# Kernel optimization log

Hardware: AMD Instinct MI355X
Metric: run time of the kernel (lower is better)

Reference implementation:

```python
import jax, jax.numpy as jnp
import numpy as np

N, IN_DIM, OUT_DIM = 8192, 512, 256


def setup_inputs() -> dict:
    key = jax.random.key(0)
    k1, k2, k3 = jax.random.split(key, 3)
    X = jax.random.normal(k1, (N, IN_DIM), dtype=jnp.float32)
    # torch nn.Linear(in_dim, out_dim, bias=False): y = x @ W^T; store as [in_dim, out_dim]
    W = jax.random.normal(k2, (IN_DIM, OUT_DIM), dtype=jnp.float32) / np.sqrt(IN_DIM)
    # a: Linear(2*out_dim, 1, bias=False) -> vector of length 2*out_dim
    a = jax.random.normal(k3, (2 * OUT_DIM,), dtype=jnp.float32) / np.sqrt(2 * OUT_DIM)
    return {"X": X, "W": W, "a": a}


def reference(X, W, a):
    H = X @ W  # [N, D]
    D = H.shape[1]
    # a([Hi ; Hj]) = Hi @ a[:D] + Hj @ a[D:] -> avoid materializing [N,N,2D]
    e = (H @ a[:D])[:, None] + (H @ a[D:])[None, :]  # [N, N]
    e = jnp.where(e > 0, e, 0.2 * e)  # leaky_relu(0.2)
    A = jax.nn.softmax(e, axis=-1)  # row softmax [N, N]
    out = A @ H  # [N, D]
    return out, A
```

## Files before the change

kernel.cpp:

```cpp
#include <hip/hip_runtime.h>
#include <math.h>

#define NN 8192
#define KDIM 512
#define DD 256
#define CS 32
#define NC 256

typedef float4 f4;
typedef __attribute__((ext_vector_type(4))) float f4v;

__device__ __forceinline__ float dot4(const f4& x, const f4& y) {
  return x.x * y.x + x.y * y.y + x.z * y.z + x.w * y.w;
}

__global__ __launch_bounds__(256) void k_gemm(const float* __restrict__ X,
                                              const float* __restrict__ W,
                                              const float* __restrict__ av,
                                              float* __restrict__ H,
                                              float* __restrict__ s,
                                              float* __restrict__ t) {
  __shared__ float Xs[32][64];
  __shared__ float Ws[32][64];
  const int tid = threadIdx.x;
  const int tx = tid & 15;
  const int ty = tid >> 4;
  const int r0 = blockIdx.x * 64;
  const int c0 = blockIdx.y * 64;
  float acc[4][4] = {};
  for (int k0 = 0; k0 < KDIM; k0 += 32) {
#pragma unroll
    for (int q = 0; q < 2; ++q) {
      int fi = tid + q * 256;
      int r = fi >> 3;
      int kq = fi & 7;
      f4 v = *reinterpret_cast<const f4*>(&X[(size_t)(r0 + r) * KDIM + k0 + kq * 4]);
      Xs[kq * 4 + 0][r] = v.x; Xs[kq * 4 + 1][r] = v.y;
      Xs[kq * 4 + 2][r] = v.z; Xs[kq * 4 + 3][r] = v.w;
    }
#pragma unroll
    for (int q = 0; q < 2; ++q) {
      int fi = tid + q * 256;
      int k = fi >> 4;
      int cq = fi & 15;
      *reinterpret_cast<f4*>(&Ws[k][cq * 4]) =
          *reinterpret_cast<const f4*>(&W[(size_t)(k0 + k) * DD + c0 + cq * 4]);
    }
    __syncthreads();
#pragma unroll
    for (int k = 0; k < 32; ++k) {
      f4 xv = *reinterpret_cast<const f4*>(&Xs[k][ty * 4]);
      f4 wv = *reinterpret_cast<const f4*>(&Ws[k][tx * 4]);
      float xs[4] = {xv.x, xv.y, xv.z, xv.w};
      float ws[4] = {wv.x, wv.y, wv.z, wv.w};
#pragma unroll
      for (int i = 0; i < 4; ++i)
#pragma unroll
        for (int j = 0; j < 4; ++j) acc[i][j] += xs[i] * ws[j];
    }
    __syncthreads();
  }
#pragma unroll
  for (int i = 0; i < 4; ++i) {
    f4 v = {acc[i][0], acc[i][1], acc[i][2], acc[i][3]};
    *reinterpret_cast<f4*>(&H[(size_t)(r0 + ty * 4 + i) * DD + c0 + tx * 4]) = v;
  }

  if (c0 == 0) {
    int wid = tid >> 6, lane = tid & 63;
    float* wv1 = &Xs[0][0];
    float* wv2 = &Xs[0][0] + 512;
    for (int k = tid; k < KDIM; k += 256) {
      float a1acc = 0.f, a2acc = 0.f;
#pragma unroll 8
      for (int d4 = 0; d4 < DD / 4; ++d4) {
        f4 wrow = *reinterpret_cast<const f4*>(&W[(size_t)k * DD + d4 * 4]);
        f4 a1v = *reinterpret_cast<const f4*>(&av[d4 * 4]);
        f4 a2v = *reinterpret_cast<const f4*>(&av[DD + d4 * 4]);
        a1acc += dot4(wrow, a1v);
        a2acc += dot4(wrow, a2v);
      }
      wv1[k] = a1acc;
      wv2[k] = a2acc;
    }
    __syncthreads();
    f4 w1a = *reinterpret_cast<const f4*>(&wv1[lane * 8]);
    f4 w1b = *reinterpret_cast<const f4*>(&wv1[lane * 8 + 4]);
    f4 w2a = *reinterpret_cast<const f4*>(&wv2[lane * 8]);
    f4 w2b = *reinterpret_cast<const f4*>(&wv2[lane * 8 + 4]);
    for (int rr = 0; rr < 16; ++rr) {
      int i = r0 + wid * 16 + rr;
      f4 xa = *reinterpret_cast<const f4*>(&X[(size_t)i * KDIM + lane * 8]);
      f4 xb = *reinterpret_cast<const f4*>(&X[(size_t)i * KDIM + lane * 8 + 4]);
      float p1 = dot4(xa, w1a) + dot4(xb, w1b);
      float p2 = dot4(xa, w2a) + dot4(xb, w2b);
      for (int off = 32; off > 0; off >>= 1) {
        p1 += __shfl_down(p1, off);
        p2 += __shfl_down(p2, off);
      }
      if (lane == 0) { s[i] = p1; t[i] = p2; }
    }
  }
}

__global__ __launch_bounds__(256) void k_mid(const float* __restrict__ s,
                                             const float* __restrict__ t,
                                             float* __restrict__ E1,
                                             float* __restrict__ E2,
                                             float* __restrict__ c1,
                                             float* __restrict__ c2,
                                             float* __restrict__ tsort,
                                             int* __restrict__ perm,
                                             float* __restrict__ Es1,
                                             float* __restrict__ Es2,
                                             int* __restrict__ kidx) {
  __shared__ float lred[4];
  const int b = blockIdx.x, tid = threadIdx.x;
  const int wid = tid >> 6, lane = tid & 63;
  float m = -1e30f;
#pragma unroll
  for (int q = 0; q < 8; ++q) {
    int idx = (q * 256 + tid) * 4;
    f4 v = *reinterpret_cast<const f4*>(&t[idx]);
    m = fmaxf(m, fmaxf(fmaxf(v.x, v.y), fmaxf(v.z, v.w)));
  }
  for (int off = 32; off > 0; off >>= 1) m = fmaxf(m, __shfl_down(m, off));
  if (lane == 0) lred[wid] = m;
  __syncthreads();
  float tmax = fmaxf(fmaxf(lred[0], lred[1]), fmaxf(lred[2], lred[3]));

  if (tid < 16) {
    int i = b * 16 + tid;
    float ti = t[i];
    E1[i] = expf(ti);
    E2[i] = expf(0.2f * ti);
    float si = s[i];
    float e = si + tmax;
    float mm = e > 0.f ? e : 0.2f * e;
    c1[i] = expf(si - mm);
    c2[i] = expf(0.2f * si - mm);
  }

  float tkv[4], skv[4]; int jj[4], cnt[4], cntk[4];
#pragma unroll
  for (int q = 0; q < 4; ++q) {
    jj[q] = b * 16 + wid * 4 + q;
    tkv[q] = t[jj[q]];
    skv[q] = -s[jj[q]];
    cnt[q] = 0;
    cntk[q] = 0;
  }
  for (int m2 = 0; m2 < 32; ++m2) {
    int i4 = m2 * 64 + lane;
    f4 v = *reinterpret_cast<const f4*>(&t[i4 * 4]);
    int base = i4 * 4;
#pragma unroll
    for (int q = 0; q < 4; ++q) {
      cnt[q] += (v.x < tkv[q]) || (v.x == tkv[q] && base + 0 < jj[q]);
      cnt[q] += (v.y < tkv[q]) || (v.y == tkv[q] && base + 1 < jj[q]);
      cnt[q] += (v.z < tkv[q]) || (v.z == tkv[q] && base + 2 < jj[q]);
      cnt[q] += (v.w < tkv[q]) || (v.w == tkv[q] && base + 3 < jj[q]);
      cntk[q] += (v.x <= skv[q]) + (v.y <= skv[q]) + (v.z <= skv[q]) + (v.w <= skv[q]);
    }
  }
#pragma unroll
  for (int q = 0; q < 4; ++q) {
    int c = cnt[q], ck = cntk[q];
    for (int off = 32; off > 0; off >>= 1) {
      c += __shfl_down(c, off);
      ck += __shfl_down(ck, off);
    }
    if (lane == 0) {
      tsort[c] = tkv[q];
      perm[c] = jj[q];
      Es1[c] = expf(tkv[q]);
      Es2[c] = expf(0.2f * tkv[q]);
      kidx[jj[q]] = ck;
    }
  }
}

__global__ __launch_bounds__(256) void k_chunk(const float* __restrict__ H,
                                               const float* __restrict__ Es1,
                                               const float* __restrict__ Es2,
                                               const int* __restrict__ perm,
                                               float* __restrict__ Hs,
                                               float* __restrict__ Ctot1,
                                               float* __restrict__ Ctot2,
                                               float* __restrict__ cs1,
                                               float* __restrict__ cs2) {
  __shared__ int pms[CS];
  int c = blockIdx.x;
  int d = threadIdx.x;
  if (d < CS) pms[d] = perm[c * CS + d];
  __syncthreads();
  float s1 = 0.f, s2 = 0.f, a1 = 0.f, a2 = 0.f;
#pragma unroll 4
  for (int kk = 0; kk < CS; ++kk) {
    int mI = c * CS + kk;
    float e1 = Es1[mI], e2 = Es2[mI];
    float h = H[(size_t)pms[kk] * DD + d];
    Hs[(size_t)mI * DD + d] = h;
    s1 += e1 * h; s2 += e2 * h;
    a1 += e1;     a2 += e2;
  }
  Ctot1[c * DD + d] = s1;
  Ctot2[c * DD + d] = s2;
  if (d == 0) { cs1[c] = a1; cs2[c] = a2; }
}

__global__ __launch_bounds__(256) void k_scan(const float* __restrict__ Ctot1,
                                              const float* __restrict__ Ctot2,
                                              const float* __restrict__ cs1,
                                              const float* __restrict__ cs2,
                                              const float* __restrict__ Es1,
                                              const float* __restrict__ Es2,
                                              const int* __restrict__ kidx,
                                              const float* __restrict__ c1,
                                              const float* __restrict__ c2,
                                              float* __restrict__ Cpre1,
                                              float* __restrict__ Cpre2,
                                              float* __restrict__ f1,
                                              float* __restrict__ f2) {
  __shared__ float sc1[NC], sc2[NC];
  const int c = blockIdx.x;
  const int d = threadIdx.x;
  float r1a = 0.f, r1b = 0.f, r2a = 0.f, r2b = 0.f;
  int cc = 0;
  for (; cc + 4 <= c; cc += 4) {
    r1a += Ctot1[(cc + 0) * DD + d];
    r1b += Ctot1[(cc + 1) * DD + d];
    r1a += Ctot1[(cc + 2) * DD + d];
    r1b += Ctot1[(cc + 3) * DD + d];
    r2a += Ctot2[(cc + 0) * DD + d];
    r2b += Ctot2[(cc + 1) * DD + d];
    r2a += Ctot2[(cc + 2) * DD + d];
    r2b += Ctot2[(cc + 3) * DD + d];
  }
  for (; cc < c; ++cc) {
    r1a += Ctot1[cc * DD + d];
    r2a += Ctot2[cc * DD + d];
  }
  float r1 = r1a + r1b, r2 = r2a + r2b;
  Cpre1[(size_t)c * DD + d] = r1;
  Cpre2[(size_t)c * DD + d] = r2;
  if (c == NC - 1) {
    Cpre1[(size_t)NC * DD + d] = r1 + Ctot1[c * DD + d];
    Cpre2[(size_t)NC * DD + d] = r2 + Ctot2[c * DD + d];
  }
  sc1[d] = cs1[d];
  sc2[d] = cs2[d];
  __syncthreads();
  for (int off = 1; off < NC; off <<= 1) {
    float y1 = (d >= off) ? sc1[d - off] : 0.f;
    float y2 = (d >= off) ? sc2[d - off] : 0.f;
    __syncthreads();
    sc1[d] += y1; sc2[d] += y2;
    __syncthreads();
  }
  if (d < 32) {
    int i = c * 32 + d;
    int ki = kidx[i];
    int ci = ki >> 5;
    float sp1 = ci ? sc1[ci - 1] : 0.f;
    float sp2 = ci ? sc2[ci - 1] : 0.f;
    for (int m = ci * CS; m < ki; ++m) { sp1 += Es1[m]; sp2 += Es2[m]; }
    float T1s = sc1[NC - 1];
    float a1 = c1[i], a2 = c2[i];
    float Z = a1 * (T1s - sp1) + a2 * sp2;
    float rZ = 1.0f / Z;
    f1[i] = rZ * a1;
    f2[i] = rZ * a2;
  }
}

__global__ __launch_bounds__(256) void k_fin2(const int* __restrict__ kidx,
                                              const float* __restrict__ Es1,
                                              const float* __restrict__ Es2,
                                              const float* __restrict__ Hs,
                                              const float* __restrict__ Cpre1,
                                              const float* __restrict__ Cpre2,
                                              const float* __restrict__ f1,
                                              const float* __restrict__ f2,
                                              float* __restrict__ out) {
  const int b = blockIdx.x;
  const int d = threadIdx.x;
  float T1 = Cpre1[(size_t)NC * DD + d];
#pragma unroll
  for (int r = 0; r < 4; ++r) {
    int i = b * 4 + r;
    int ki = kidx[i];
    int ci = ki >> 5;
    float P1 = Cpre1[(size_t)ci * DD + d];
    float P2 = Cpre2[(size_t)ci * DD + d];
    for (int m = ci * CS; m < ki; ++m) {
      float h = Hs[(size_t)m * DD + d];
      P1 += Es1[m] * h;
      P2 += Es2[m] * h;
    }
    out[(size_t)i * DD + d] = f1[i] * (T1 - P1) + f2[i] * P2;
  }
}

__global__ __launch_bounds__(256) void k_astream(const float* __restrict__ s,
                                                 const float* __restrict__ t,
                                                 const float* __restrict__ E1,
                                                 const float* __restrict__ E2,
                                                 const float* __restrict__ f1,
                                                 const float* __restrict__ f2,
                                                 float* __restrict__ A) {
  int j0 = blockIdx.x * 1024 + threadIdx.x * 4;
  int i0 = blockIdx.y * 32;
  f4 t4  = *reinterpret_cast<const f4*>(&t[j0]);
  f4 e14 = *reinterpret_cast<const f4*>(&E1[j0]);
  f4 e24 = *reinterpret_cast<const f4*>(&E2[j0]);
#pragma unroll 4
  for (int rr = 0; rr < 32; ++rr) {
    int i = i0 + rr;
    float ss = s[i], ff1 = f1[i], ff2 = f2[i];
    f4v o;
    float e;
    e = ss + t4.x; o.x = (e > 0.f) ? ff1 * e14.x : ff2 * e24.x;
    e = ss + t4.y; o.y = (e > 0.f) ? ff1 * e14.y : ff2 * e24.y;
    e = ss + t4.z; o.z = (e > 0.f) ? ff1 * e14.z : ff2 * e24.z;
    e = ss + t4.w; o.w = (e > 0.f) ? ff1 * e14.w : ff2 * e24.w;
    __builtin_nontemporal_store(o, reinterpret_cast<f4v*>(&A[(size_t)i * NN + j0]));
  }
}

extern "C" void kernel_launch(void* const* d_in, const int* in_sizes, int n_in,
                              void* d_out, int out_size, void* d_ws, size_t ws_size,
                              hipStream_t stream) {
  const float* X  = (const float*)d_in[0];
  const float* W  = (const float*)d_in[1];
  const float* av = (const float*)d_in[2];
  float* outp = (float*)d_out;
  float* A = outp + (size_t)NN * DD;

  float* wsp = (float*)d_ws;
  float* s  = wsp + 0 * NN;
  float* t  = wsp + 1 * NN;
  float* E1 = wsp + 2 * NN;
  float* E2 = wsp + 3 * NN;
  float* c1 = wsp + 4 * NN;
  float* c2 = wsp + 5 * NN;
  float* f1 = wsp + 6 * NN;
  float* f2 = wsp + 7 * NN;

  float* Ctot1 = A;
  float* Ctot2 = A + 65536;
  float* Cpre1 = A + 131072;
  float* Cpre2 = A + 196864;
  float* cs1   = A + 262656;
  float* cs2   = A + 262912;
  float* tsort = A + 263168;
  int*   perm  = (int*)(A + 271360);
  int*   kidx  = (int*)(A + 279552);
  float* Es1   = A + 287744;
  float* Es2   = A + 295936;
  float* H     = A + 16777216;
  float* Hs    = A + 20971520;

  k_gemm<<<dim3(NN / 64, DD / 64), 256, 0, stream>>>(X, W, av, H, s, t);
  k_mid<<<NN / 16, 256, 0, stream>>>(s, t, E1, E2, c1, c2, tsort, perm,
                                     Es1, Es2, kidx);
  k_chunk<<<NC, 256, 0, stream>>>(H, Es1, Es2, perm, Hs, Ctot1, Ctot2, cs1, cs2);
  k_scan<<<NC, 256, 0, stream>>>(Ctot1, Ctot2, cs1, cs2, Es1, Es2, kidx, c1, c2,
                                 Cpre1, Cpre2, f1, f2);
  k_fin2<<<NN / 4, 256, 0, stream>>>(kidx, Es1, Es2, Hs, Cpre1, Cpre2, f1, f2, outp);
  k_astream<<<dim3(NN / 1024, NN / 32), 256, 0, stream>>>(s, t, E1, E2, f1, f2, A);
}
```

Measured before the change: 197.6 us.

## Fuse final output and attention-matrix stream kernels, drop sorted H copy

Removes the permuted copy Hs and the unused tsort writes, so the final pass gathers H rows through perm instead. When the workspace is large enough, scratch buffers move from the A output region into the workspace, which lets the output-row computation and the A-matrix streaming store run in a single fused kernel. The goal is to cut an 8 MB copy and one launch, and to overlap the gather-heavy output rows with the bandwidth-bound A stream. The cost is indirect, less coalesced H reads in the tail loop, plus an unfused fallback path when the workspace is small.

```diff
diff --git a/kernel.cpp b/kernel.cpp
--- a/kernel.cpp
+++ b/kernel.cpp
@@ -109,7 +109,6 @@
                                              float* __restrict__ E2,
                                              float* __restrict__ c1,
                                              float* __restrict__ c2,
-                                             float* __restrict__ tsort,
                                              int* __restrict__ perm,
                                              float* __restrict__ Es1,
                                              float* __restrict__ Es2,
@@ -171,7 +170,6 @@
       ck += __shfl_down(ck, off);
     }
     if (lane == 0) {
-      tsort[c] = tkv[q];
       perm[c] = jj[q];
       Es1[c] = expf(tkv[q]);
       Es2[c] = expf(0.2f * tkv[q]);
@@ -184,7 +182,6 @@
                                                const float* __restrict__ Es1,
                                                const float* __restrict__ Es2,
                                                const int* __restrict__ perm,
-                                               float* __restrict__ Hs,
                                                float* __restrict__ Ctot1,
                                                float* __restrict__ Ctot2,
                                                float* __restrict__ cs1,
@@ -200,7 +197,6 @@
     int mI = c * CS + kk;
     float e1 = Es1[mI], e2 = Es2[mI];
     float h = H[(size_t)pms[kk] * DD + d];
-    Hs[(size_t)mI * DD + d] = h;
     s1 += e1 * h; s2 += e2 * h;
     a1 += e1;     a2 += e2;
   }
@@ -274,27 +270,27 @@
   }
 }
 
-__global__ __launch_bounds__(256) void k_fin2(const int* __restrict__ kidx,
-                                              const float* __restrict__ Es1,
-                                              const float* __restrict__ Es2,
-                                              const float* __restrict__ Hs,
-                                              const float* __restrict__ Cpre1,
-                                              const float* __restrict__ Cpre2,
-                                              const float* __restrict__ f1,
-                                              const float* __restrict__ f2,
-                                              float* __restrict__ out) {
-  const int b = blockIdx.x;
-  const int d = threadIdx.x;
+__device__ __forceinline__ void fin_rows(int i0, int d,
+                                         const int* __restrict__ kidx,
+                                         const float* __restrict__ Es1,
+                                         const float* __restrict__ Es2,
+                                         const int* __restrict__ perm,
+                                         const float* __restrict__ H,
+                                         const float* __restrict__ Cpre1,
+                                         const float* __restrict__ Cpre2,
+                                         const float* __restrict__ f1,
+                                         const float* __restrict__ f2,
+                                         float* __restrict__ out) {
   float T1 = Cpre1[(size_t)NC * DD + d];
 #pragma unroll
   for (int r = 0; r < 4; ++r) {
-    int i = b * 4 + r;
+    int i = i0 + r;
     int ki = kidx[i];
     int ci = ki >> 5;
     float P1 = Cpre1[(size_t)ci * DD + d];
     float P2 = Cpre2[(size_t)ci * DD + d];
     for (int m = ci * CS; m < ki; ++m) {
-      float h = Hs[(size_t)m * DD + d];
+      float h = H[(size_t)perm[m] * DD + d];
       P1 += Es1[m] * h;
       P2 += Es2[m] * h;
     }
@@ -302,15 +298,14 @@
   }
 }
 
-__global__ __launch_bounds__(256) void k_astream(const float* __restrict__ s,
-                                                 const float* __restrict__ t,
-                                                 const float* __restrict__ E1,
-                                                 const float* __restrict__ E2,
-                                                 const float* __restrict__ f1,
-                                                 const float* __restrict__ f2,
-                                                 float* __restrict__ A) {
-  int j0 = blockIdx.x * 1024 + threadIdx.x * 4;
-  int i0 = blockIdx.y * 32;
+__device__ __forceinline__ void astream_tile(int i0, int j0,
+                                             const float* __restrict__ s,
+                                             const float* __restrict__ t,
+                                             const float* __restrict__ E1,
+                                             const float* __restrict__ E2,
+                                             const float* __restrict__ f1,
+                                             const float* __restrict__ f2,
+                                             float* __restrict__ A) {
   f4 t4  = *reinterpret_cast<const f4*>(&t[j0]);
   f4 e14 = *reinterpret_cast<const f4*>(&E1[j0]);
   f4 e24 = *reinterpret_cast<const f4*>(&E2[j0]);
@@ -328,6 +323,52 @@
   }
 }
 
+__global__ __launch_bounds__(256) void k_finstream(const int* __restrict__ kidx,
+                                                   const float* __restrict__ Es1,
+                                                   const float* __restrict__ Es2,
+                                                   const int* __restrict__ perm,
+                                                   const float* __restrict__ H,
+                                                   const float* __restrict__ Cpre1,
+                                                   const float* __restrict__ Cpre2,
+                                                   const float* __restrict__ f1,
+                                                   const float* __restrict__ f2,
+                                                   float* __restrict__ out,
+                                                   const float* __restrict__ s,
+                                                   const float* __restrict__ t,
+                                                   const float* __restrict__ E1,
+                                                   const float* __restrict__ E2,
+                                                   float* __restrict__ A) {
+  const int bb = blockIdx.x;
+  const int d = threadIdx.x;
+  fin_rows(bb * 4, d, kidx, Es1, Es2, perm, H, Cpre1, Cpre2, f1, f2, out);
+  astream_tile((bb >> 3) * 32, (bb & 7) * 1024 + d * 4, s, t, E1, E2, f1, f2, A);
+}
+
+__global__ __launch_bounds__(256) void k_fin2(const int* __restrict__ kidx,
+                                              const float* __restrict__ Es1,
+                                              const float* __restrict__ Es2,
+                                              const int* __restrict__ perm,
+                                              const float* __restrict__ H,
+                                              const float* __restrict__ Cpre1,
+                                              const float* __restrict__ Cpre2,
+                                              const float* __restrict__ f1,
+                                              const float* __restrict__ f2,
+                                              float* __restrict__ out) {
+  fin_rows(blockIdx.x * 4, threadIdx.x, kidx, Es1, Es2, perm, H, Cpre1, Cpre2,
+           f1, f2, out);
+}
+
+__global__ __launch_bounds__(256) void k_astream(const float* __restrict__ s,
+                                                 const float* __restrict__ t,
+                                                 const float* __restrict__ E1,
+                                                 const float* __restrict__ E2,
+                                                 const float* __restrict__ f1,
+                                                 const float* __restrict__ f2,
+                                                 float* __restrict__ A) {
+  astream_tile(blockIdx.y * 32, blockIdx.x * 1024 + threadIdx.x * 4,
+               s, t, E1, E2, f1, f2, A);
+}
+
 extern "C" void kernel_launch(void* const* d_in, const int* in_sizes, int n_in,
                               void* d_out, int out_size, void* d_ws, size_t ws_size,
                               hipStream_t stream) {
@@ -336,8 +377,8 @@
   const float* av = (const float*)d_in[2];
   float* outp = (float*)d_out;
   float* A = outp + (size_t)NN * DD;
-
   float* wsp = (float*)d_ws;
+
   float* s  = wsp + 0 * NN;
   float* t  = wsp + 1 * NN;
   float* E1 = wsp + 2 * NN;
@@ -347,26 +388,47 @@
   float* f1 = wsp + 6 * NN;
   float* f2 = wsp + 7 * NN;
 
-  float* Ctot1 = A;
-  float* Ctot2 = A + 65536;
-  float* Cpre1 = A + 131072;
-  float* Cpre2 = A + 196864;
-  float* cs1   = A + 262656;
-  float* cs2   = A + 262912;
-  float* tsort = A + 263168;
-  int*   perm  = (int*)(A + 271360);
-  int*   kidx  = (int*)(A + 279552);
-  float* Es1   = A + 287744;
-  float* Es2   = A + 295936;
-  float* H     = A + 16777216;
-  float* Hs    = A + 20971520;
-
-  k_gemm<<<dim3(NN / 64, DD / 64), 256, 0, stream>>>(X, W, av, H, s, t);
-  k_mid<<<NN / 16, 256, 0, stream>>>(s, t, E1, E2, c1, c2, tsort, perm,
-                                     Es1, Es2, kidx);
-  k_chunk<<<NC, 256, 0, stream>>>(H, Es1, Es2, perm, Hs, Ctot1, Ctot2, cs1, cs2);
-  k_scan<<<NC, 256, 0, stream>>>(Ctot1, Ctot2, cs1, cs2, Es1, Es2, kidx, c1, c2,
-                                 Cpre1, Cpre2, f1, f2);
-  k_fin2<<<NN / 4, 256, 0, stream>>>(kidx, Es1, Es2, Hs, Cpre1, Cpre2, f1, f2, outp);
-  k_astream<<<dim3(NN / 1024, NN / 32), 256, 0, stream>>>(s, t, E1, E2, f1, f2, A);
-}
+  const size_t FAST_WS_FLOATS = 393216 + (size_t)NN * DD;
+  if (ws_size >= FAST_WS_FLOATS * sizeof(float)) {
+    float* Ctot1 = wsp + 65536;
+    float* Ctot2 = wsp + 131072;
+    float* Cpre1 = wsp + 196608;
+    float* Cpre2 = wsp + 262400;
+    float* cs1   = wsp + 328192;
+    float* cs2   = wsp + 328448;
+    float* Es1   = wsp + 328704;
+    float* Es2   = wsp + 336896;
+    int*   kidx  = (int*)(wsp + 345088);
+    int*   perm  = (int*)(wsp + 353280);
+    float* H     = wsp + 393216;
+
+    k_gemm<<<dim3(NN / 64, DD / 64), 256, 0, stream>>>(X, W, av, H, s, t);
+    k_mid<<<NN / 16, 256, 0, stream>>>(s, t, E1, E2, c1, c2, perm, Es1, Es2, kidx);
+    k_chunk<<<NC, 256, 0, stream>>>(H, Es1, Es2, perm, Ctot1, Ctot2, cs1, cs2);
+    k_scan<<<NC, 256, 0, stream>>>(Ctot1, Ctot2, cs1, cs2, Es1, Es2, kidx, c1, c2,
+                                   Cpre1, Cpre2, f1, f2);
+    k_finstream<<<NN / 4, 256, 0, stream>>>(kidx, Es1, Es2, perm, H, Cpre1, Cpre2,
+                                            f1, f2, outp, s, t, E1, E2, A);
+  } else {
+    float* Ctot1 = A;
+    float* Ctot2 = A + 65536;
+    float* Cpre1 = A + 131072;
+    float* Cpre2 = A + 196864;
+    float* cs1   = A + 262656;
+    float* cs2   = A + 262912;
+    int*   perm  = (int*)(A + 271360);
+    int*   kidx  = (int*)(A + 279552);
+    float* Es1   = A + 287744;
+    float* Es2   = A + 295936;
+    float* H     = A + 16777216;
+
+    k_gemm<<<dim3(NN / 64, DD / 64), 256, 0, stream>>>(X, W, av, H, s, t);
+    k_mid<<<NN / 16, 256, 0, stream>>>(s, t, E1, E2, c1, c2, perm, Es1, Es2, kidx);
+    k_chunk<<<NC, 256, 0, stream>>>(H, Es1, Es2, perm, Ctot1, Ctot2, cs1, cs2);
+    k_scan<<<NC, 256, 0, stream>>>(Ctot1, Ctot2, cs1, cs2, Es1, Es2, kidx, c1, c2,
+                                   Cpre1, Cpre2, f1, f2);
+    k_fin2<<<NN / 4, 256, 0, stream>>>(kidx, Es1, Es2, perm, H, Cpre1, Cpre2,
+                                       f1, f2, outp);
+    k_astream<<<dim3(NN / 1024, NN / 32), 256, 0, stream>>>(s, t, E1, E2, f1, f2, A);
+  }
+}
```

Result: faster. 183.5 us (median of 2 runs) (-7.2%).

## Replace rank-count sort with value-bucketed histogram and fuse output with A stream

Applied to the files above, without the earlier changes.

Swaps the O(N^2) rank-counting sort of t for value-range bucketing into 256 buckets, each sorted locally by one block from a shared-memory copy of t. The same block also gathers H and computes per-bucket weighted totals, merging the old mid and chunk kernels. The output-row kernel and the A-writing stream kernel become one launch, and scratch moves from the A region into the workspace. Bucket sizes now depend on the data, so a skewed distribution can overflow the 2048-entry bucket list and cause uneven per-block work.

```diff
diff --git a/kernel.cpp b/kernel.cpp
--- a/kernel.cpp
+++ b/kernel.cpp
@@ -4,14 +4,18 @@
 #define NN 8192
 #define KDIM 512
 #define DD 256
-#define CS 32
-#define NC 256
+#define NCB 256
 
 typedef float4 f4;
 typedef __attribute__((ext_vector_type(4))) float f4v;
 
 __device__ __forceinline__ float dot4(const f4& x, const f4& y) {
   return x.x * y.x + x.y * y.y + x.z * y.z + x.w * y.w;
+}
+
+__device__ __forceinline__ int bk(float x, float tmin, float sc) {
+  int b = (int)floorf((x - tmin) * sc);
+  return b < 0 ? 0 : (b > NCB - 1 ? NCB - 1 : b);
 }
 
 __global__ __launch_bounds__(256) void k_gemm(const float* __restrict__ X,
@@ -103,35 +107,59 @@
   }
 }
 
-__global__ __launch_bounds__(256) void k_mid(const float* __restrict__ s,
-                                             const float* __restrict__ t,
-                                             float* __restrict__ E1,
-                                             float* __restrict__ E2,
-                                             float* __restrict__ c1,
-                                             float* __restrict__ c2,
-                                             float* __restrict__ tsort,
-                                             int* __restrict__ perm,
-                                             float* __restrict__ Es1,
-                                             float* __restrict__ Es2,
-                                             int* __restrict__ kidx) {
-  __shared__ float lred[4];
-  const int b = blockIdx.x, tid = threadIdx.x;
+__global__ __launch_bounds__(256) void k_vtot(const float* __restrict__ s,
+                                              const float* __restrict__ t,
+                                              const float* __restrict__ H,
+                                              float* __restrict__ E1,
+                                              float* __restrict__ E2,
+                                              float* __restrict__ c1,
+                                              float* __restrict__ c2,
+                                              float* __restrict__ Vtot1,
+                                              float* __restrict__ Vtot2,
+                                              float* __restrict__ Vcs1,
+                                              float* __restrict__ Vcs2,
+                                              float* __restrict__ tz,
+                                              float* __restrict__ Ez1,
+                                              float* __restrict__ Ez2,
+                                              float* __restrict__ Hs,
+                                              int* __restrict__ boffg,
+                                              int* __restrict__ cntg,
+                                              float* __restrict__ tmm) {
+  __shared__ float ts[NN];
+  __shared__ int hist[NCB];
+  __shared__ int sh1[NCB];
+  __shared__ int tcnt[256];
+  __shared__ int sh2[256];
+  __shared__ int mlist[2048];
+  __shared__ int srt[2048];
+  __shared__ float lred[4], lredn[4];
+  const int c = blockIdx.x, tid = threadIdx.x;
   const int wid = tid >> 6, lane = tid & 63;
-  float m = -1e30f;
+
+  float mx = -1e30f, mn = 1e30f;
 #pragma unroll
   for (int q = 0; q < 8; ++q) {
     int idx = (q * 256 + tid) * 4;
     f4 v = *reinterpret_cast<const f4*>(&t[idx]);
-    m = fmaxf(m, fmaxf(fmaxf(v.x, v.y), fmaxf(v.z, v.w)));
-  }
-  for (int off = 32; off > 0; off >>= 1) m = fmaxf(m, __shfl_down(m, off));
-  if (lane == 0) lred[wid] = m;
+    *reinterpret_cast<f4*>(&ts[idx]) = v;
+    mx = fmaxf(mx, fmaxf(fmaxf(v.x, v.y), fmaxf(v.z, v.w)));
+    mn = fminf(mn, fminf(fminf(v.x, v.y), fminf(v.z, v.w)));
+  }
+  for (int off = 32; off > 0; off >>= 1) {
+    mx = fmaxf(mx, __shfl_down(mx, off));
+    mn = fminf(mn, __shfl_down(mn, off));
+  }
+  if (lane == 0) { lred[wid] = mx; lredn[wid] = mn; }
   __syncthreads();
   float tmax = fmaxf(fmaxf(lred[0], lred[1]), fmaxf(lred[2], lred[3]));
-
-  if (tid < 16) {
-    int i = b * 16 + tid;
-    float ti = t[i];
+  float tmin = fminf(fminf(lredn[0], lredn[1]), fminf(lredn[2], lredn[3]));
+  float range = tmax - tmin;
+  float sc = (range > 0.f) ? (float)NCB / range : 0.f;
+  if (c == 0 && tid == 0) { tmm[0] = tmin; tmm[1] = sc; }
+
+  if (tid < 32) {
+    int i = c * 32 + tid;
+    float ti = ts[i];
     E1[i] = expf(ti);
     E2[i] = expf(0.2f * ti);
     float si = s[i];
@@ -141,117 +169,125 @@
     c2[i] = expf(0.2f * si - mm);
   }
 
-  float tkv[4], skv[4]; int jj[4], cnt[4], cntk[4];
-#pragma unroll
-  for (int q = 0; q < 4; ++q) {
-    jj[q] = b * 16 + wid * 4 + q;
-    tkv[q] = t[jj[q]];
-    skv[q] = -s[jj[q]];
-    cnt[q] = 0;
-    cntk[q] = 0;
-  }
-  for (int m2 = 0; m2 < 32; ++m2) {
-    int i4 = m2 * 64 + lane;
-    f4 v = *reinterpret_cast<const f4*>(&t[i4 * 4]);
-    int base = i4 * 4;
-#pragma unroll
-    for (int q = 0; q < 4; ++q) {
-      cnt[q] += (v.x < tkv[q]) || (v.x == tkv[q] && base + 0 < jj[q]);
-      cnt[q] += (v.y < tkv[q]) || (v.y == tkv[q] && base + 1 < jj[q]);
-      cnt[q] += (v.z < tkv[q]) || (v.z == tkv[q] && base + 2 < jj[q]);
-      cnt[q] += (v.w < tkv[q]) || (v.w == tkv[q] && base + 3 < jj[q]);
-      cntk[q] += (v.x <= skv[q]) + (v.y <= skv[q]) + (v.z <= skv[q]) + (v.w <= skv[q]);
-    }
-  }
-#pragma unroll
-  for (int q = 0; q < 4; ++q) {
-    int c = cnt[q], ck = cntk[q];
-    for (int off = 32; off > 0; off >>= 1) {
-      c += __shfl_down(c, off);
-      ck += __shfl_down(ck, off);
-    }
-    if (lane == 0) {
-      tsort[c] = tkv[q];
-      perm[c] = jj[q];
-      Es1[c] = expf(tkv[q]);
-      Es2[c] = expf(0.2f * tkv[q]);
-      kidx[jj[q]] = ck;
-    }
-  }
-}
-
-__global__ __launch_bounds__(256) void k_chunk(const float* __restrict__ H,
-                                               const float* __restrict__ Es1,
-                                               const float* __restrict__ Es2,
-                                               const int* __restrict__ perm,
-                                               float* __restrict__ Hs,
-                                               float* __restrict__ Ctot1,
-                                               float* __restrict__ Ctot2,
-                                               float* __restrict__ cs1,
-                                               float* __restrict__ cs2) {
-  __shared__ int pms[CS];
-  int c = blockIdx.x;
-  int d = threadIdx.x;
-  if (d < CS) pms[d] = perm[c * CS + d];
-  __syncthreads();
-  float s1 = 0.f, s2 = 0.f, a1 = 0.f, a2 = 0.f;
-#pragma unroll 4
-  for (int kk = 0; kk < CS; ++kk) {
-    int mI = c * CS + kk;
-    float e1 = Es1[mI], e2 = Es2[mI];
-    float h = H[(size_t)pms[kk] * DD + d];
-    Hs[(size_t)mI * DD + d] = h;
-    s1 += e1 * h; s2 += e2 * h;
-    a1 += e1;     a2 += e2;
-  }
-  Ctot1[c * DD + d] = s1;
-  Ctot2[c * DD + d] = s2;
-  if (d == 0) { cs1[c] = a1; cs2[c] = a2; }
-}
-
-__global__ __launch_bounds__(256) void k_scan(const float* __restrict__ Ctot1,
-                                              const float* __restrict__ Ctot2,
-                                              const float* __restrict__ cs1,
-                                              const float* __restrict__ cs2,
-                                              const float* __restrict__ Es1,
-                                              const float* __restrict__ Es2,
-                                              const int* __restrict__ kidx,
+  hist[tid] = 0;
+  __syncthreads();
+  int myc = 0;
+  for (int k = 0; k < 32; ++k) {
+    int j = tid * 32 + k;
+    int b = bk(ts[j], tmin, sc);
+    atomicAdd(&hist[b], 1);
+    myc += (b == c);
+  }
+  tcnt[tid] = myc;
+  __syncthreads();
+  int h0 = hist[tid], tc0 = tcnt[tid];
+  sh1[tid] = h0; sh2[tid] = tc0;
+  __syncthreads();
+  for (int off = 1; off < 256; off <<= 1) {
+    int a1 = (tid >= off) ? sh1[tid - off] : 0;
+    int a2 = (tid >= off) ? sh2[tid - off] : 0;
+    __syncthreads();
+    sh1[tid] += a1; sh2[tid] += a2;
+    __syncthreads();
+  }
+  const int boffc = (c > 0) ? sh1[c - 1] : 0;
+  const int nm = hist[c];
+  const int tb = sh2[tid] - tc0;
+  if (tid == 0) { boffg[c] = boffc; cntg[c] = nm; }
+
+  int w = 0;
+  for (int k = 0; k < 32; ++k) {
+    int j = tid * 32 + k;
+    if (bk(ts[j], tmin, sc) == c) {
+      int slot = tb + w;
+      if (slot < 2048) mlist[slot] = j;
+      ++w;
+    }
+  }
+  __syncthreads();
+
+  for (int k = tid; k < nm; k += 256) {
+    int j = mlist[k];
+    float v = ts[j];
+    int r = 0;
+    for (int k2 = 0; k2 < nm; ++k2) {
+      int j2 = mlist[k2];
+      float v2 = ts[j2];
+      r += (v2 < v) || (v2 == v && j2 < j);
+    }
+    srt[r] = j;
+  }
+  __syncthreads();
+
+  float a1 = 0.f, a2 = 0.f, scs1 = 0.f, scs2 = 0.f;
+  for (int r2 = 0; r2 < nm; ++r2) {
+    int j = srt[r2];
+    float tv = ts[j];
+    float e1 = expf(tv), e2 = expf(0.2f * tv);
+    float hv = H[(size_t)j * DD + tid];
+    Hs[(size_t)(boffc + r2) * DD + tid] = hv;
+    a1 += e1 * hv;
+    a2 += e2 * hv;
+    if (tid == 0) {
+      tz[boffc + r2] = tv;
+      Ez1[boffc + r2] = e1;
+      Ez2[boffc + r2] = e2;
+      scs1 += e1;
+      scs2 += e2;
+    }
+  }
+  Vtot1[c * DD + tid] = a1;
+  Vtot2[c * DD + tid] = a2;
+  if (tid == 0) { Vcs1[c] = scs1; Vcs2[c] = scs2; }
+}
+
+__global__ __launch_bounds__(256) void k_scan(const float* __restrict__ Vtot1,
+                                              const float* __restrict__ Vtot2,
+                                              const float* __restrict__ Vcs1,
+                                              const float* __restrict__ Vcs2,
+                                              const float* __restrict__ tz,
+                                              const float* __restrict__ Ez1,
+                                              const float* __restrict__ Ez2,
+                                              const int* __restrict__ boffg,
+                                              const int* __restrict__ cntg,
+                                              const float* __restrict__ tmm,
+                                              const float* __restrict__ s,
                                               const float* __restrict__ c1,
                                               const float* __restrict__ c2,
-                                              float* __restrict__ Cpre1,
-                                              float* __restrict__ Cpre2,
+                                              float* __restrict__ Vpre1,
+                                              float* __restrict__ Vpre2,
                                               float* __restrict__ f1,
                                               float* __restrict__ f2) {
-  __shared__ float sc1[NC], sc2[NC];
+  __shared__ float sc1[NCB], sc2[NCB];
   const int c = blockIdx.x;
   const int d = threadIdx.x;
   float r1a = 0.f, r1b = 0.f, r2a = 0.f, r2b = 0.f;
   int cc = 0;
   for (; cc + 4 <= c; cc += 4) {
-    r1a += Ctot1[(cc + 0) * DD + d];
-    r1b += Ctot1[(cc + 1) * DD + d];
-    r1a += Ctot1[(cc + 2) * DD + d];
-    r1b += Ctot1[(cc + 3) * DD + d];
-    r2a += Ctot2[(cc + 0) * DD + d];
-    r2b += Ctot2[(cc + 1) * DD + d];
-    r2a += Ctot2[(cc + 2) * DD + d];
-    r2b += Ctot2[(cc + 3) * DD + d];
+    r1a += Vtot1[(cc + 0) * DD + d];
+    r1b += Vtot1[(cc + 1) * DD + d];
+    r1a += Vtot1[(cc + 2) * DD + d];
+    r1b += Vtot1[(cc + 3) * DD + d];
+    r2a += Vtot2[(cc + 0) * DD + d];
+    r2b += Vtot2[(cc + 1) * DD + d];
+    r2a += Vtot2[(cc + 2) * DD + d];
+    r2b += Vtot2[(cc + 3) * DD + d];
   }
   for (; cc < c; ++cc) {
-    r1a += Ctot1[cc * DD + d];
-    r2a += Ctot2[cc * DD + d];
+    r1a += Vtot1[cc * DD + d];
+    r2a += Vtot2[cc * DD + d];
   }
   float r1 = r1a + r1b, r2 = r2a + r2b;
-  Cpre1[(size_t)c * DD + d] = r1;
-  Cpre2[(size_t)c * DD + d] = r2;
-  if (c == NC - 1) {
-    Cpre1[(size_t)NC * DD + d] = r1 + Ctot1[c * DD + d];
-    Cpre2[(size_t)NC * DD + d] = r2 + Ctot2[c * DD + d];
-  }
-  sc1[d] = cs1[d];
-  sc2[d] = cs2[d];
-  __syncthreads();
-  for (int off = 1; off < NC; off <<= 1) {
+  Vpre1[(size_t)c * DD + d] = r1;
+  Vpre2[(size_t)c * DD + d] = r2;
+  if (c == NCB - 1) {
+    Vpre1[(size_t)NCB * DD + d] = r1 + Vtot1[c * DD + d];
+    Vpre2[(size_t)NCB * DD + d] = r2 + Vtot2[c * DD + d];
+  }
+  sc1[d] = Vcs1[d];
+  sc2[d] = Vcs2[d];
+  __syncthreads();
+  for (int off = 1; off < NCB; off <<= 1) {
     float y1 = (d >= off) ? sc1[d - off] : 0.f;
     float y2 = (d >= off) ? sc2[d - off] : 0.f;
     __syncthreads();
@@ -260,12 +296,19 @@
   }
   if (d < 32) {
     int i = c * 32 + d;
-    int ki = kidx[i];
-    int ci = ki >> 5;
-    float sp1 = ci ? sc1[ci - 1] : 0.f;
-    float sp2 = ci ? sc2[ci - 1] : 0.f;
-    for (int m = ci * CS; m < ki; ++m) { sp1 += Es1[m]; sp2 += Es2[m]; }
-    float T1s = sc1[NC - 1];
+    float th = -s[i];
+    float tmin = tmm[0], scl = tmm[1];
+    int b = bk(th, tmin, scl);
+    float sp1 = b ? sc1[b - 1] : 0.f;
+    float sp2 = b ? sc2[b - 1] : 0.f;
+    int base = boffg[b], n = cntg[b];
+    for (int k = 0; k < n; ++k) {
+      float tv = tz[base + k];
+      if (tv > th) break;
+      sp1 += Ez1[base + k];
+      sp2 += Ez2[base + k];
+    }
+    float T1s = sc1[NCB - 1];
     float a1 = c1[i], a2 = c2[i];
     float Z = a1 * (T1s - sp1) + a2 * sp2;
     float rZ = 1.0f / Z;
@@ -274,57 +317,64 @@
   }
 }
 
-__global__ __launch_bounds__(256) void k_fin2(const int* __restrict__ kidx,
-                                              const float* __restrict__ Es1,
-                                              const float* __restrict__ Es2,
-                                              const float* __restrict__ Hs,
-                                              const float* __restrict__ Cpre1,
-                                              const float* __restrict__ Cpre2,
-                                              const float* __restrict__ f1,
-                                              const float* __restrict__ f2,
-                                              float* __restrict__ out) {
-  const int b = blockIdx.x;
+__global__ __launch_bounds__(256) void k_finstream(const float* __restrict__ s,
+                                                   const float* __restrict__ t,
+                                                   const float* __restrict__ E1,
+                                                   const float* __restrict__ E2,
+                                                   const float* __restrict__ f1,
+                                                   const float* __restrict__ f2,
+                                                   const float* __restrict__ tz,
+                                                   const float* __restrict__ Ez1,
+                                                   const float* __restrict__ Ez2,
+                                                   const float* __restrict__ Hs,
+                                                   const float* __restrict__ Vpre1,
+                                                   const float* __restrict__ Vpre2,
+                                                   const int* __restrict__ boffg,
+                                                   const int* __restrict__ cntg,
+                                                   const float* __restrict__ tmm,
+                                                   float* __restrict__ out,
+                                                   float* __restrict__ A) {
+  const int bb = blockIdx.x;
   const int d = threadIdx.x;
-  float T1 = Cpre1[(size_t)NC * DD + d];
-#pragma unroll
-  for (int r = 0; r < 4; ++r) {
-    int i = b * 4 + r;
-    int ki = kidx[i];
-    int ci = ki >> 5;
-    float P1 = Cpre1[(size_t)ci * DD + d];
-    float P2 = Cpre2[(size_t)ci * DD + d];
-    for (int m = ci * CS; m < ki; ++m) {
-      float h = Hs[(size_t)m * DD + d];
-      P1 += Es1[m] * h;
-      P2 += Es2[m] * h;
-    }
-    out[(size_t)i * DD + d] = f1[i] * (T1 - P1) + f2[i] * P2;
-  }
-}
-
-__global__ __launch_bounds__(256) void k_astream(const float* __restrict__ s,
-                                                 const float* __restrict__ t,
-                                                 const float* __restrict__ E1,
-                                                 const float* __restrict__ E2,
-                                                 const float* __restrict__ f1,
-                                                 const float* __restrict__ f2,
-                                                 float* __restrict__ A) {
-  int j0 = blockIdx.x * 1024 + threadIdx.x * 4;
-  int i0 = blockIdx.y * 32;
-  f4 t4  = *reinterpret_cast<const f4*>(&t[j0]);
-  f4 e14 = *reinterpret_cast<const f4*>(&E1[j0]);
-  f4 e24 = *reinterpret_cast<const f4*>(&E2[j0]);
+  {
+    float tmin = tmm[0], scl = tmm[1];
+    float T1 = Vpre1[(size_t)NCB * DD + d];
+#pragma unroll
+    for (int r = 0; r < 4; ++r) {
+      int i = bb * 4 + r;
+      float th = -s[i];
+      int b = bk(th, tmin, scl);
+      int base = boffg[b], n = cntg[b];
+      float P1 = Vpre1[(size_t)b * DD + d];
+      float P2 = Vpre2[(size_t)b * DD + d];
+      for (int k = 0; k < n; ++k) {
+        float tv = tz[base + k];
+        if (tv > th) break;
+        float hv = Hs[(size_t)(base + k) * DD + d];
+        P1 += Ez1[base + k] * hv;
+        P2 += Ez2[base + k] * hv;
+      }
+      out[(size_t)i * DD + d] = f1[i] * (T1 - P1) + f2[i] * P2;
+    }
+  }
+  {
+    int i0 = (bb >> 3) * 32;
+    int j0 = (bb & 7) * 1024 + d * 4;
+    f4 t4  = *reinterpret_cast<const f4*>(&t[j0]);
+    f4 e14 = *reinterpret_cast<const f4*>(&E1[j0]);
+    f4 e24 = *reinterpret_cast<const f4*>(&E2[j0]);
 #pragma unroll 4
-  for (int rr = 0; rr < 32; ++rr) {
-    int i = i0 + rr;
-    float ss = s[i], ff1 = f1[i], ff2 = f2[i];
-    f4v o;
-    float e;
-    e = ss + t4.x; o.x = (e > 0.f) ? ff1 * e14.x : ff2 * e24.x;
-    e = ss + t4.y; o.y = (e > 0.f) ? ff1 * e14.y : ff2 * e24.y;
-    e = ss + t4.z; o.z = (e > 0.f) ? ff1 * e14.z : ff2 * e24.z;
-    e = ss + t4.w; o.w = (e > 0.f) ? ff1 * e14.w : ff2 * e24.w;
-    __builtin_nontemporal_store(o, reinterpret_cast<f4v*>(&A[(size_t)i * NN + j0]));
+    for (int rr = 0; rr < 32; ++rr) {
+      int i = i0 + rr;
+      float ss = s[i], ff1 = f1[i], ff2 = f2[i];
+      f4v o;
+      float e;
+      e = ss + t4.x; o.x = (e > 0.f) ? ff1 * e14.x : ff2 * e24.x;
+      e = ss + t4.y; o.y = (e > 0.f) ? ff1 * e14.y : ff2 * e24.y;
+      e = ss + t4.z; o.z = (e > 0.f) ? ff1 * e14.z : ff2 * e24.z;
+      e = ss + t4.w; o.w = (e > 0.f) ? ff1 * e14.w : ff2 * e24.w;
+      __builtin_nontemporal_store(o, reinterpret_cast<f4v*>(&A[(size_t)i * NN + j0]));
+    }
   }
 }
 
@@ -336,37 +386,39 @@
   const float* av = (const float*)d_in[2];
   float* outp = (float*)d_out;
   float* A = outp + (size_t)NN * DD;
-
   float* wsp = (float*)d_ws;
-  float* s  = wsp + 0 * NN;
-  float* t  = wsp + 1 * NN;
-  float* E1 = wsp + 2 * NN;
-  float* E2 = wsp + 3 * NN;
-  float* c1 = wsp + 4 * NN;
-  float* c2 = wsp + 5 * NN;
-  float* f1 = wsp + 6 * NN;
-  float* f2 = wsp + 7 * NN;
-
-  float* Ctot1 = A;
-  float* Ctot2 = A + 65536;
-  float* Cpre1 = A + 131072;
-  float* Cpre2 = A + 196864;
-  float* cs1   = A + 262656;
-  float* cs2   = A + 262912;
-  float* tsort = A + 263168;
-  int*   perm  = (int*)(A + 271360);
-  int*   kidx  = (int*)(A + 279552);
-  float* Es1   = A + 287744;
-  float* Es2   = A + 295936;
-  float* H     = A + 16777216;
-  float* Hs    = A + 20971520;
+
+  float* s     = wsp + 0;
+  float* t     = wsp + 8192;
+  float* E1    = wsp + 16384;
+  float* E2    = wsp + 24576;
+  float* c1    = wsp + 32768;
+  float* c2    = wsp + 40960;
+  float* f1    = wsp + 49152;
+  float* f2    = wsp + 57344;
+  float* Vtot1 = wsp + 65536;
+  float* Vtot2 = wsp + 131072;
+  float* Vpre1 = wsp + 196608;
+  float* Vpre2 = wsp + 262400;
+  float* Vcs1  = wsp + 328192;
+  float* Vcs2  = wsp + 328448;
+  float* tz    = wsp + 328704;
+  float* Ez1   = wsp + 336896;
+  float* Ez2   = wsp + 345088;
+  int*   boffg = (int*)(wsp + 353280);
+  int*   cntg  = (int*)(wsp + 353536);
+  float* tmm   = wsp + 353792;
+  float* Hs    = wsp + 360448;
+
+  float* H = A;
 
   k_gemm<<<dim3(NN / 64, DD / 64), 256, 0, stream>>>(X, W, av, H, s, t);
-  k_mid<<<NN / 16, 256, 0, stream>>>(s, t, E1, E2, c1, c2, tsort, perm,
-                                     Es1, Es2, kidx);
-  k_chunk<<<NC, 256, 0, stream>>>(H, Es1, Es2, perm, Hs, Ctot1, Ctot2, cs1, cs2);
-  k_scan<<<NC, 256, 0, stream>>>(Ctot1, Ctot2, cs1, cs2, Es1, Es2, kidx, c1, c2,
-                                 Cpre1, Cpre2, f1, f2);
-  k_fin2<<<NN / 4, 256, 0, stream>>>(kidx, Es1, Es2, Hs, Cpre1, Cpre2, f1, f2, outp);
-  k_astream<<<dim3(NN / 1024, NN / 32), 256, 0, stream>>>(s, t, E1, E2, f1, f2, A);
-}
+  k_vtot<<<NCB, 256, 0, stream>>>(s, t, H, E1, E2, c1, c2, Vtot1, Vtot2,
+                                  Vcs1, Vcs2, tz, Ez1, Ez2, Hs, boffg, cntg, tmm);
+  k_scan<<<NCB, 256, 0, stream>>>(Vtot1, Vtot2, Vcs1, Vcs2, tz, Ez1, Ez2,
+                                  boffg, cntg, tmm, s, c1, c2,
+                                  Vpre1, Vpre2, f1, f2);
+  k_finstream<<<NN / 4, 256, 0, stream>>>(s, t, E1, E2, f1, f2, tz, Ez1, Ez2,
+                                          Hs, Vpre1, Vpre2, boffg, cntg, tmm,
+                                          outp, A);
+}
```

Result: slower. 268.0 us (+35.6%).

## Fuse chunk sums into sort kernel via atomics and merge output with A-stream

Applied to the files above, without the earlier changes.

Removes the k_chunk kernel: k_mid now scatters exp-weighted H rows into per-chunk sums with atomicAdd, and the zeroing of those accumulators is folded into the GEMM kernel. The sorted copy Hs is no longer materialized; the final kernel gathers H through perm instead. The output computation and the A-matrix streaming are merged into one launch, and scratch buffers move from the A region to workspace. This trades two launches and an 8 MB copy for float atomics, nondeterministic summation order and scattered gathers.

```diff
diff --git a/kernel.cpp b/kernel.cpp
--- a/kernel.cpp
+++ b/kernel.cpp
@@ -19,7 +19,9 @@
                                               const float* __restrict__ av,
                                               float* __restrict__ H,
                                               float* __restrict__ s,
-                                              float* __restrict__ t) {
+                                              float* __restrict__ t,
+                                              float* __restrict__ Ctot1,
+                                              float* __restrict__ cs1) {
   __shared__ float Xs[32][64];
   __shared__ float Ws[32][64];
   const int tid = threadIdx.x;
@@ -27,6 +29,15 @@
   const int ty = tid >> 4;
   const int r0 = blockIdx.x * 64;
   const int c0 = blockIdx.y * 64;
+
+  if (blockIdx.y == 1) {
+    f4 z = {0.f, 0.f, 0.f, 0.f};
+    *reinterpret_cast<f4*>(&Ctot1[blockIdx.x * 1024 + tid * 4]) = z;
+  } else if (blockIdx.y == 2 && blockIdx.x == 0 && tid < 128) {
+    f4 z = {0.f, 0.f, 0.f, 0.f};
+    *reinterpret_cast<f4*>(&cs1[tid * 4]) = z;
+  }
+
   float acc[4][4] = {};
   for (int k0 = 0; k0 < KDIM; k0 += 32) {
 #pragma unroll
@@ -105,16 +116,22 @@
 
 __global__ __launch_bounds__(256) void k_mid(const float* __restrict__ s,
                                              const float* __restrict__ t,
+                                             const float* __restrict__ H,
                                              float* __restrict__ E1,
                                              float* __restrict__ E2,
                                              float* __restrict__ c1,
                                              float* __restrict__ c2,
-                                             float* __restrict__ tsort,
                                              int* __restrict__ perm,
                                              float* __restrict__ Es1,
                                              float* __restrict__ Es2,
-                                             int* __restrict__ kidx) {
+                                             int* __restrict__ kidx,
+                                             float* __restrict__ Ctot1,
+                                             float* __restrict__ Ctot2,
+                                             float* __restrict__ cs1,
+                                             float* __restrict__ cs2) {
   __shared__ float lred[4];
+  __shared__ int   kJ[16], kC[16];
+  __shared__ float kE1[16], kE2[16];
   const int b = blockIdx.x, tid = threadIdx.x;
   const int wid = tid >> 6, lane = tid & 63;
   float m = -1e30f;
@@ -171,42 +188,27 @@
       ck += __shfl_down(ck, off);
     }
     if (lane == 0) {
-      tsort[c] = tkv[q];
+      float e1 = expf(tkv[q]);
+      float e2 = expf(0.2f * tkv[q]);
       perm[c] = jj[q];
-      Es1[c] = expf(tkv[q]);
-      Es2[c] = expf(0.2f * tkv[q]);
+      Es1[c] = e1;
+      Es2[c] = e2;
       kidx[jj[q]] = ck;
-    }
-  }
-}
-
-__global__ __launch_bounds__(256) void k_chunk(const float* __restrict__ H,
-                                               const float* __restrict__ Es1,
-                                               const float* __restrict__ Es2,
-                                               const int* __restrict__ perm,
-                                               float* __restrict__ Hs,
-                                               float* __restrict__ Ctot1,
-                                               float* __restrict__ Ctot2,
-                                               float* __restrict__ cs1,
-                                               float* __restrict__ cs2) {
-  __shared__ int pms[CS];
-  int c = blockIdx.x;
-  int d = threadIdx.x;
-  if (d < CS) pms[d] = perm[c * CS + d];
+      int cc = c >> 5;
+      int idx = wid * 4 + q;
+      kJ[idx] = jj[q]; kC[idx] = cc; kE1[idx] = e1; kE2[idx] = e2;
+      atomicAdd(&cs1[cc], e1);
+      atomicAdd(&cs2[cc], e2);
+    }
+  }
   __syncthreads();
-  float s1 = 0.f, s2 = 0.f, a1 = 0.f, a2 = 0.f;
-#pragma unroll 4
-  for (int kk = 0; kk < CS; ++kk) {
-    int mI = c * CS + kk;
-    float e1 = Es1[mI], e2 = Es2[mI];
-    float h = H[(size_t)pms[kk] * DD + d];
-    Hs[(size_t)mI * DD + d] = h;
-    s1 += e1 * h; s2 += e2 * h;
-    a1 += e1;     a2 += e2;
-  }
-  Ctot1[c * DD + d] = s1;
-  Ctot2[c * DD + d] = s2;
-  if (d == 0) { cs1[c] = a1; cs2[c] = a2; }
+#pragma unroll
+  for (int q = 0; q < 16; ++q) {
+    int j = kJ[q], cc = kC[q];
+    float h = H[(size_t)j * DD + tid];
+    atomicAdd(&Ctot1[cc * DD + tid], kE1[q] * h);
+    atomicAdd(&Ctot2[cc * DD + tid], kE2[q] * h);
+  }
 }
 
 __global__ __launch_bounds__(256) void k_scan(const float* __restrict__ Ctot1,
@@ -274,57 +276,58 @@
   }
 }
 
-__global__ __launch_bounds__(256) void k_fin2(const int* __restrict__ kidx,
-                                              const float* __restrict__ Es1,
-                                              const float* __restrict__ Es2,
-                                              const float* __restrict__ Hs,
-                                              const float* __restrict__ Cpre1,
-                                              const float* __restrict__ Cpre2,
-                                              const float* __restrict__ f1,
-                                              const float* __restrict__ f2,
-                                              float* __restrict__ out) {
-  const int b = blockIdx.x;
+__global__ __launch_bounds__(256) void k_finstream(const int* __restrict__ kidx,
+                                                   const float* __restrict__ Es1,
+                                                   const float* __restrict__ Es2,
+                                                   const int* __restrict__ perm,
+                                                   const float* __restrict__ H,
+                                                   const float* __restrict__ Cpre1,
+                                                   const float* __restrict__ Cpre2,
+                                                   const float* __restrict__ f1,
+                                                   const float* __restrict__ f2,
+                                                   float* __restrict__ out,
+                                                   const float* __restrict__ s,
+                                                   const float* __restrict__ t,
+                                                   const float* __restrict__ E1,
+                                                   const float* __restrict__ E2,
+                                                   float* __restrict__ A) {
+  const int bb = blockIdx.x;
   const int d = threadIdx.x;
-  float T1 = Cpre1[(size_t)NC * DD + d];
-#pragma unroll
-  for (int r = 0; r < 4; ++r) {
-    int i = b * 4 + r;
-    int ki = kidx[i];
-    int ci = ki >> 5;
-    float P1 = Cpre1[(size_t)ci * DD + d];
-    float P2 = Cpre2[(size_t)ci * DD + d];
-    for (int m = ci * CS; m < ki; ++m) {
-      float h = Hs[(size_t)m * DD + d];
-      P1 += Es1[m] * h;
-      P2 += Es2[m] * h;
-    }
-    out[(size_t)i * DD + d] = f1[i] * (T1 - P1) + f2[i] * P2;
-  }
-}
-
-__global__ __launch_bounds__(256) void k_astream(const float* __restrict__ s,
-                                                 const float* __restrict__ t,
-                                                 const float* __restrict__ E1,
-                                                 const float* __restrict__ E2,
-                                                 const float* __restrict__ f1,
-                                                 const float* __restrict__ f2,
-                                                 float* __restrict__ A) {
-  int j0 = blockIdx.x * 1024 + threadIdx.x * 4;
-  int i0 = blockIdx.y * 32;
-  f4 t4  = *reinterpret_cast<const f4*>(&t[j0]);
-  f4 e14 = *reinterpret_cast<const f4*>(&E1[j0]);
-  f4 e24 = *reinterpret_cast<const f4*>(&E2[j0]);
+  {
+    float T1 = Cpre1[(size_t)NC * DD + d];
+#pragma unroll
+    for (int r = 0; r < 4; ++r) {
+      int i = bb * 4 + r;
+      int ki = kidx[i];
+      int ci = ki >> 5;
+      float P1 = Cpre1[(size_t)ci * DD + d];
+      float P2 = Cpre2[(size_t)ci * DD + d];
+      for (int m = ci * CS; m < ki; ++m) {
+        float h = H[(size_t)perm[m] * DD + d];
+        P1 += Es1[m] * h;
+        P2 += Es2[m] * h;
+      }
+      out[(size_t)i * DD + d] = f1[i] * (T1 - P1) + f2[i] * P2;
+    }
+  }
+  {
+    int i0 = (bb >> 3) * 32;
+    int j0 = (bb & 7) * 1024 + d * 4;
+    f4 t4  = *reinterpret_cast<const f4*>(&t[j0]);
+    f4 e14 = *reinterpret_cast<const f4*>(&E1[j0]);
+    f4 e24 = *reinterpret_cast<const f4*>(&E2[j0]);
 #pragma unroll 4
-  for (int rr = 0; rr < 32; ++rr) {
-    int i = i0 + rr;
-    float ss = s[i], ff1 = f1[i], ff2 = f2[i];
-    f4v o;
-    float e;
-    e = ss + t4.x; o.x = (e > 0.f) ? ff1 * e14.x : ff2 * e24.x;
-    e = ss + t4.y; o.y = (e > 0.f) ? ff1 * e14.y : ff2 * e24.y;
-    e = ss + t4.z; o.z = (e > 0.f) ? ff1 * e14.z : ff2 * e24.z;
-    e = ss + t4.w; o.w = (e > 0.f) ? ff1 * e14.w : ff2 * e24.w;
-    __builtin_nontemporal_store(o, reinterpret_cast<f4v*>(&A[(size_t)i * NN + j0]));
+    for (int rr = 0; rr < 32; ++rr) {
+      int i = i0 + rr;
+      float ss = s[i], ff1 = f1[i], ff2 = f2[i];
+      f4v o;
+      float e;
+      e = ss + t4.x; o.x = (e > 0.f) ? ff1 * e14.x : ff2 * e24.x;
+      e = ss + t4.y; o.y = (e > 0.f) ? ff1 * e14.y : ff2 * e24.y;
+      e = ss + t4.z; o.z = (e > 0.f) ? ff1 * e14.z : ff2 * e24.z;
+      e = ss + t4.w; o.w = (e > 0.f) ? ff1 * e14.w : ff2 * e24.w;
+      __builtin_nontemporal_store(o, reinterpret_cast<f4v*>(&A[(size_t)i * NN + j0]));
+    }
   }
 }
 
@@ -336,37 +339,33 @@
   const float* av = (const float*)d_in[2];
   float* outp = (float*)d_out;
   float* A = outp + (size_t)NN * DD;
-
   float* wsp = (float*)d_ws;
-  float* s  = wsp + 0 * NN;
-  float* t  = wsp + 1 * NN;
-  float* E1 = wsp + 2 * NN;
-  float* E2 = wsp + 3 * NN;
-  float* c1 = wsp + 4 * NN;
-  float* c2 = wsp + 5 * NN;
-  float* f1 = wsp + 6 * NN;
-  float* f2 = wsp + 7 * NN;
-
-  float* Ctot1 = A;
-  float* Ctot2 = A + 65536;
-  float* Cpre1 = A + 131072;
-  float* Cpre2 = A + 196864;
-  float* cs1   = A + 262656;
-  float* cs2   = A + 262912;
-  float* tsort = A + 263168;
-  int*   perm  = (int*)(A + 271360);
-  int*   kidx  = (int*)(A + 279552);
-  float* Es1   = A + 287744;
-  float* Es2   = A + 295936;
-  float* H     = A + 16777216;
-  float* Hs    = A + 20971520;
-
-  k_gemm<<<dim3(NN / 64, DD / 64), 256, 0, stream>>>(X, W, av, H, s, t);
-  k_mid<<<NN / 16, 256, 0, stream>>>(s, t, E1, E2, c1, c2, tsort, perm,
-                                     Es1, Es2, kidx);
-  k_chunk<<<NC, 256, 0, stream>>>(H, Es1, Es2, perm, Hs, Ctot1, Ctot2, cs1, cs2);
+
+  float* s     = wsp + 0;
+  float* t     = wsp + 8192;
+  float* E1    = wsp + 16384;
+  float* E2    = wsp + 24576;
+  float* c1    = wsp + 32768;
+  float* c2    = wsp + 40960;
+  float* f1    = wsp + 49152;
+  float* f2    = wsp + 57344;
+  float* Ctot1 = wsp + 65536;
+  float* Ctot2 = wsp + 131072;
+  float* Cpre1 = wsp + 196608;
+  float* Cpre2 = wsp + 262400;
+  float* cs1   = wsp + 328192;
+  float* cs2   = wsp + 328448;
+  float* Es1   = wsp + 328704;
+  float* Es2   = wsp + 336896;
+  int*   kidx  = (int*)(wsp + 345088);
+  int*   perm  = (int*)(wsp + 353280);
+  float* H     = wsp + 393216;
+
+  k_gemm<<<dim3(NN / 64, DD / 64), 256, 0, stream>>>(X, W, av, H, s, t, Ctot1, cs1);
+  k_mid<<<NN / 16, 256, 0, stream>>>(s, t, H, E1, E2, c1, c2, perm, Es1, Es2,
+                                     kidx, Ctot1, Ctot2, cs1, cs2);
   k_scan<<<NC, 256, 0, stream>>>(Ctot1, Ctot2, cs1, cs2, Es1, Es2, kidx, c1, c2,
                                  Cpre1, Cpre2, f1, f2);
-  k_fin2<<<NN / 4, 256, 0, stream>>>(kidx, Es1, Es2, Hs, Cpre1, Cpre2, f1, f2, outp);
-  k_astream<<<dim3(NN / 1024, NN / 32), 256, 0, stream>>>(s, t, E1, E2, f1, f2, A);
-}
+  k_finstream<<<NN / 4, 256, 0, stream>>>(kidx, Es1, Es2, perm, H, Cpre1, Cpre2,
+                                          f1, f2, outp, s, t, E1, E2, A);
+}
```

Result: slower. 202.6 us (+2.6%).
